# Performance work log

Measured on AMD Instinct MI355X. Metric: run time of the kernel, lower is better.

Reference implementation:

```python
import jax, jax.numpy as jnp
import numpy as np

HEAD_DIM = 64
SCALE = 1.0 / np.sqrt(HEAD_DIM).astype(np.float32)


def setup_inputs() -> dict:
    key = jax.random.key(0)
    k1, k2 = jax.random.split(key)
    B, S, D = 4, 4096, 1024
    x = jax.random.normal(k1, (B, S, D), dtype=jnp.float32)
    wq = jax.random.normal(k2, (HEAD_DIM, D), dtype=jnp.float32) * (1.0 / np.sqrt(D))
    return {"x": x, "wq": wq}


def reference(x, wq):
    # Faithful to the original forward: wq is (buggily) used for q, k AND v.
    q = jnp.einsum('bsd,hd->bsh', x, wq)   # [B, S, 64]
    k = q
    v = q
    scores = jnp.einsum('bqh,bkh->bqk', q, k) * SCALE  # [B, S, S]
    attn = jax.nn.softmax(scores, axis=-1)
    out = jnp.einsum('bqk,bkh->bqh', attn, v)          # [B, S, 64]
    return out
```

## Files before the change

### kernel.cpp

```cpp
#include <hip/hip_runtime.h>
#include <hip/hip_bf16.h>

#define B_ 4
#define S_ 4096
#define D_ 1024
#define H_ 64
#define SCALE_ 0.125f
#define CFAC_ 0.180336884f
#define WP_ 1056
#define SP_ 4224
#define NSPLIT 4

typedef __attribute__((ext_vector_type(8))) short bf16x8;
typedef __attribute__((ext_vector_type(4))) float f32x4;

static __device__ __forceinline__ short f2bf(float f) {
    unsigned u = __builtin_bit_cast(unsigned, f);
    u += 0x7fffu + ((u >> 16) & 1u);
    return (short)(u >> 16);
}

static __device__ __forceinline__ unsigned pk_trunc(float f0, float f1) {
    return (__builtin_bit_cast(unsigned, f1) & 0xffff0000u)
         | (__builtin_bit_cast(unsigned, f0) >> 16);
}

__global__ __launch_bounds__(256) void winit_kernel(
    const float* __restrict__ wq, short* __restrict__ wqb)
{
    const int i   = blockIdx.x * 256 + threadIdx.x;
    const int row = i >> 7;
    const int col = (i & 127) * 8;
    const float* s = wq + (size_t)row * D_ + col;
    bf16x8 v;
#pragma unroll
    for (int e = 0; e < 8; ++e) v[e] = f2bf(s[e]);
    *(bf16x8*)(wqb + (size_t)row * WP_ + col) = v;
}

__global__ __launch_bounds__(256) void qproj_mfma(
    const float* __restrict__ x, const short* __restrict__ wqb,
    short* __restrict__ q, short* __restrict__ qT, short* __restrict__ qsb)
{
    __shared__ short xs[4][16][264];
    __shared__ float cs[4][16][68];
    __shared__ short qs[16][68];

    const int tid  = threadIdx.x;
    const int wave = tid >> 6;
    const int lane = tid & 63;
    const int quad = lane >> 4;
    const int lr   = lane & 15;
    const int row0 = blockIdx.x * 16;

    {
        const float* xp = x + (size_t)row0 * D_ + wave * 256 + lane * 4;
#pragma unroll
        for (int s = 0; s < 16; ++s) {
            const f32x4 v = *(const f32x4*)(xp + (size_t)s * D_);
            unsigned long long pk = 0;
#pragma unroll
            for (int e = 0; e < 4; ++e)
                pk |= (unsigned long long)(unsigned short)f2bf(v[e]) << (16 * e);
            *(unsigned long long*)&xs[wave][s][lane * 4] = pk;
        }
    }
    __syncthreads();

    f32x4 acc[4];
#pragma unroll
    for (int nb = 0; nb < 4; ++nb) acc[nb] = (f32x4){0.f, 0.f, 0.f, 0.f};

    const short* wp = wqb + (size_t)lr * WP_ + wave * 256 + quad * 8;
#pragma unroll
    for (int t = 0; t < 8; ++t) {
        const bf16x8 a = *(const bf16x8*)&xs[wave][lr][t * 32 + quad * 8];
#pragma unroll
        for (int nb = 0; nb < 4; ++nb) {
            const bf16x8 bb = *(const bf16x8*)(wp + (size_t)(nb * 16) * WP_ + t * 32);
            acc[nb] = __builtin_amdgcn_mfma_f32_16x16x32_bf16(a, bb, acc[nb], 0, 0, 0);
        }
    }

#pragma unroll
    for (int nb = 0; nb < 4; ++nb)
#pragma unroll
        for (int i = 0; i < 4; ++i)
            cs[wave][quad * 4 + i][nb * 16 + lr] = acc[nb][i];
    __syncthreads();

    const int r  = tid >> 4;
    const int c4 = (tid & 15) * 4;
    unsigned long long pv = 0, pw = 0;
#pragma unroll
    for (int j = 0; j < 4; ++j) {
        const float s = cs[0][r][c4 + j] + cs[1][r][c4 + j]
                      + cs[2][r][c4 + j] + cs[3][r][c4 + j];
        pv |= (unsigned long long)(unsigned short)f2bf(s) << (16 * j);
        pw |= (unsigned long long)(unsigned short)f2bf(s * CFAC_) << (16 * j);
    }
    *(unsigned long long*)(q   + (size_t)(row0 + r) * H_ + c4) = pv;
    *(unsigned long long*)(qsb + (size_t)(row0 + r) * H_ + c4) = pw;
    *(unsigned long long*)&qs[r][c4] = pv;
    __syncthreads();

    const int hh = tid >> 2;
    const int sj = (tid & 3) * 4;
    const int b  = row0 >> 12;
    const int sl = row0 & (S_ - 1);
    unsigned long long w = 0;
#pragma unroll
    for (int e = 0; e < 4; ++e)
        w |= (unsigned long long)(unsigned short)qs[sj + e][hh] << (16 * e);
    *(unsigned long long*)(qT + ((size_t)b * H_ + hh) * SP_ + sl + sj) = w;
}

__global__ __launch_bounds__(256, 4) void flash_mfma(
    const short* __restrict__ q, const short* __restrict__ qT,
    const short* __restrict__ qsb,
    float* __restrict__ opart, float* __restrict__ lbuf)
{
    __shared__ short kt[64 * 64];
    __shared__ short vt[64 * 64];
    __shared__ short plT[4][16][72];

    const int tid  = threadIdx.x;
    const int w    = tid >> 6;
    const int lane = tid & 63;
    const int quad = lane >> 4;
    const int lr   = lane & 15;
    const int b    = blockIdx.y;
    const int q0   = blockIdx.x * 64;
    const int z    = blockIdx.z;
    const int slice = S_ / gridDim.z;
    const int kbase = z * slice;
    const short* qb  = q  + (size_t)b * S_ * H_;
    const short* qTb = qT + (size_t)b * H_ * SP_;

    bf16x8 qB[2];
    {
        const short* qr = qsb + (size_t)(b * S_ + q0 + w * 16 + lr) * H_;
        qB[0] = *(const bf16x8*)(qr + quad * 8);
        qB[1] = *(const bf16x8*)(qr + 32 + quad * 8);
    }

    bf16x8 ones;
#pragma unroll
    for (int e = 0; e < 8; ++e) ones[e] = (short)0x3f80;

    f32x4 o[4];
#pragma unroll
    for (int mt = 0; mt < 4; ++mt) o[mt] = (f32x4){0.f, 0.f, 0.f, 0.f};
    f32x4 lsum = (f32x4){0.f, 0.f, 0.f, 0.f};

    const int srow = tid >> 2;
    const int g0   = (tid & 3) * 2;
    const int sw0  = (g0 ^ (srow & 7)) * 8;
    const int sw1  = ((g0 + 1) ^ (srow & 7)) * 8;
    const short* gk = qb  + (size_t)(kbase + srow) * H_ + g0 * 8;
    const short* gv = qTb + (size_t)srow * SP_ + kbase + g0 * 8;

    uint4 pk0 = *(const uint4*)gk, pk1 = *(const uint4*)(gk + 8);
    uint4 pv0 = *(const uint4*)gv, pv1 = *(const uint4*)(gv + 8);

    const int iters = slice >> 6;
    for (int it = 0; it < iters; ++it) {
        __syncthreads();
        *(uint4*)&kt[srow * 64 + sw0] = pk0;
        *(uint4*)&kt[srow * 64 + sw1] = pk1;
        *(uint4*)&vt[srow * 64 + sw0] = pv0;
        *(uint4*)&vt[srow * 64 + sw1] = pv1;
        __syncthreads();
        if (it + 1 < iters) {
            gk += (size_t)64 * H_;
            gv += 64;
            pk0 = *(const uint4*)gk; pk1 = *(const uint4*)(gk + 8);
            pv0 = *(const uint4*)gv; pv1 = *(const uint4*)(gv + 8);
        }

        f32x4 s[4];
#pragma unroll
        for (int mt = 0; mt < 4; ++mt) s[mt] = (f32x4){0.f, 0.f, 0.f, 0.f};
#pragma unroll
        for (int c = 0; c < 2; ++c)
#pragma unroll
            for (int mt = 0; mt < 4; ++mt) {
                const int row = mt * 16 + lr;
                const bf16x8 a = *(const bf16x8*)&kt[row * 64 + (((c * 4 + quad) ^ (row & 7)) * 8)];
                s[mt] = __builtin_amdgcn_mfma_f32_16x16x32_bf16(a, qB[c], s[mt], 0, 0, 0);
            }

#pragma unroll
        for (int mt = 0; mt < 4; ++mt) {
            const float p0 = __builtin_amdgcn_exp2f(s[mt][0]);
            const float p1 = __builtin_amdgcn_exp2f(s[mt][1]);
            const float p2 = __builtin_amdgcn_exp2f(s[mt][2]);
            const float p3 = __builtin_amdgcn_exp2f(s[mt][3]);
            unsigned lohi[2];
            lohi[0] = pk_trunc(p0, p1);
            lohi[1] = pk_trunc(p2, p3);
            *(unsigned long long*)&plT[w][lr][mt * 16 + quad * 4] =
                *(unsigned long long*)lohi;
        }

#pragma unroll
        for (int c = 0; c < 2; ++c) {
            const bf16x8 pB = *(const bf16x8*)&plT[w][lr][c * 32 + quad * 8];
            lsum = __builtin_amdgcn_mfma_f32_16x16x32_bf16(ones, pB, lsum, 0, 0, 0);
#pragma unroll
            for (int mt = 0; mt < 4; ++mt) {
                const int row = mt * 16 + lr;
                const bf16x8 a = *(const bf16x8*)&vt[row * 64 + (((c * 4 + quad) ^ (row & 7)) * 8)];
                o[mt] = __builtin_amdgcn_mfma_f32_16x16x32_bf16(a, pB, o[mt], 0, 0, 0);
            }
        }
    }

    float* ob = opart + (((size_t)z * B_ + b) * S_ + q0 + w * 16 + lr) * H_;
#pragma unroll
    for (int mt = 0; mt < 4; ++mt)
        *(f32x4*)(ob + mt * 16 + quad * 4) = o[mt];
    if (quad == 0)
        lbuf[((size_t)z * B_ + b) * S_ + q0 + w * 16 + lr] = lsum[0];
}

__global__ __launch_bounds__(256) void combine_kernel(
    const float* __restrict__ opart, const float* __restrict__ lbuf,
    float* __restrict__ out, int nsplit)
{
    const int t   = blockIdx.x * 256 + threadIdx.x;
    const int row = t >> 4;
    const int c4  = (t & 15) * 4;
    f32x4 acc = (f32x4){0.f, 0.f, 0.f, 0.f};
    float l = 0.0f;
    for (int z = 0; z < nsplit; ++z) {
        const f32x4 v = *(const f32x4*)(opart + ((size_t)z * (B_ * S_) + row) * H_ + c4);
        acc[0] += v[0]; acc[1] += v[1]; acc[2] += v[2]; acc[3] += v[3];
        l += lbuf[(size_t)z * (B_ * S_) + row];
    }
    const float r = 1.0f / l;
    acc[0] *= r; acc[1] *= r; acc[2] *= r; acc[3] *= r;
    *(f32x4*)(out + (size_t)row * H_ + c4) = acc;
}

extern "C" void kernel_launch(void* const* d_in, const int* in_sizes, int n_in,
                              void* d_out, int out_size, void* d_ws, size_t ws_size,
                              hipStream_t stream) {
    const float* x  = (const float*)d_in[0];
    const float* wq = (const float*)d_in[1];
    float* out = (float*)d_out;

    const size_t off_qT  = 2097152;
    const size_t off_wqb = off_qT + (size_t)B_ * H_ * SP_ * 2;
    const size_t off_qsb = off_wqb + (size_t)H_ * WP_ * 2;
    const size_t off_op  = off_qsb + 2097152;
    short* qbuf = (short*)d_ws;
    short* qT   = (short*)((char*)d_ws + off_qT);
    short* wqb  = (short*)((char*)d_ws + off_wqb);
    short* qsb  = (short*)((char*)d_ws + off_qsb);

    const size_t per_split = (size_t)B_ * S_ * H_ * 4 + (size_t)B_ * S_ * 4;
    int nsplit = NSPLIT;
    while (nsplit > 1 && ws_size < off_op + (size_t)nsplit * per_split) nsplit >>= 1;
    float* opart = (float*)((char*)d_ws + off_op);
    float* lbuf  = (float*)((char*)d_ws + off_op + (size_t)nsplit * B_ * S_ * H_ * 4);

    winit_kernel<<<dim3(32), dim3(256), 0, stream>>>(wq, wqb);
    qproj_mfma<<<dim3((B_ * S_) / 16), dim3(256), 0, stream>>>(x, wqb, qbuf, qT, qsb);
    flash_mfma<<<dim3(S_ / 64, B_, nsplit), dim3(256), 0, stream>>>(qbuf, qT, qsb, opart, lbuf);
    combine_kernel<<<dim3(1024), dim3(256), 0, stream>>>(opart, lbuf, out, nsplit);
}
```

Before: 134.8 us.

## Process two query sub-tiles per wave to reuse K/V LDS tiles; double split count

Each flash block now covers 128 query rows instead of 64, with each wave handling two 16-row query sub-tiles that share the same K and V LDS fragments. This halves LDS loading and global K/V traffic per query row and raises the MFMA-to-load ratio. To keep the grid size the same, the key-dimension split goes from 4 to 8. That doubles the partial-output buffers and the work in the combine kernel, and the extra accumulators raise register pressure, which may hurt occupancy.

Result: no change. 134.6 us (-0.1%).

```diff
diff --git a/kernel.cpp b/kernel.cpp
--- a/kernel.cpp
+++ b/kernel.cpp
@@ -9,7 +9,7 @@
 #define CFAC_ 0.180336884f
 #define WP_ 1056
 #define SP_ 4224
-#define NSPLIT 4
+#define NSPLIT 8
 
 typedef __attribute__((ext_vector_type(8))) short bf16x8;
 typedef __attribute__((ext_vector_type(4))) float f32x4;
@@ -122,7 +122,7 @@
 {
     __shared__ short kt[64 * 64];
     __shared__ short vt[64 * 64];
-    __shared__ short plT[4][16][72];
+    __shared__ short plT[4][2][16][72];
 
     const int tid  = threadIdx.x;
     const int w    = tid >> 6;
@@ -130,28 +130,33 @@
     const int quad = lane >> 4;
     const int lr   = lane & 15;
     const int b    = blockIdx.y;
-    const int q0   = blockIdx.x * 64;
+    const int q0   = blockIdx.x * 128;
     const int z    = blockIdx.z;
     const int slice = S_ / gridDim.z;
     const int kbase = z * slice;
     const short* qb  = q  + (size_t)b * S_ * H_;
     const short* qTb = qT + (size_t)b * H_ * SP_;
 
-    bf16x8 qB[2];
-    {
-        const short* qr = qsb + (size_t)(b * S_ + q0 + w * 16 + lr) * H_;
-        qB[0] = *(const bf16x8*)(qr + quad * 8);
-        qB[1] = *(const bf16x8*)(qr + 32 + quad * 8);
+    bf16x8 qB[2][2];
+#pragma unroll
+    for (int qs = 0; qs < 2; ++qs) {
+        const short* qr = qsb + (size_t)(b * S_ + q0 + w * 32 + qs * 16 + lr) * H_;
+        qB[qs][0] = *(const bf16x8*)(qr + quad * 8);
+        qB[qs][1] = *(const bf16x8*)(qr + 32 + quad * 8);
     }
 
     bf16x8 ones;
 #pragma unroll
     for (int e = 0; e < 8; ++e) ones[e] = (short)0x3f80;
 
-    f32x4 o[4];
-#pragma unroll
-    for (int mt = 0; mt < 4; ++mt) o[mt] = (f32x4){0.f, 0.f, 0.f, 0.f};
-    f32x4 lsum = (f32x4){0.f, 0.f, 0.f, 0.f};
+    f32x4 o[2][4];
+#pragma unroll
+    for (int qs = 0; qs < 2; ++qs)
+#pragma unroll
+        for (int mt = 0; mt < 4; ++mt) o[qs][mt] = (f32x4){0.f, 0.f, 0.f, 0.f};
+    f32x4 lsum[2];
+    lsum[0] = (f32x4){0.f, 0.f, 0.f, 0.f};
+    lsum[1] = (f32x4){0.f, 0.f, 0.f, 0.f};
 
     const int srow = tid >> 2;
     const int g0   = (tid & 3) * 2;
@@ -178,50 +183,64 @@
             pv0 = *(const uint4*)gv; pv1 = *(const uint4*)(gv + 8);
         }
 
-        f32x4 s[4];
-#pragma unroll
-        for (int mt = 0; mt < 4; ++mt) s[mt] = (f32x4){0.f, 0.f, 0.f, 0.f};
-#pragma unroll
-        for (int c = 0; c < 2; ++c)
-#pragma unroll
-            for (int mt = 0; mt < 4; ++mt) {
-                const int row = mt * 16 + lr;
-                const bf16x8 a = *(const bf16x8*)&kt[row * 64 + (((c * 4 + quad) ^ (row & 7)) * 8)];
-                s[mt] = __builtin_amdgcn_mfma_f32_16x16x32_bf16(a, qB[c], s[mt], 0, 0, 0);
-            }
-
-#pragma unroll
-        for (int mt = 0; mt < 4; ++mt) {
-            const float p0 = __builtin_amdgcn_exp2f(s[mt][0]);
-            const float p1 = __builtin_amdgcn_exp2f(s[mt][1]);
-            const float p2 = __builtin_amdgcn_exp2f(s[mt][2]);
-            const float p3 = __builtin_amdgcn_exp2f(s[mt][3]);
-            unsigned lohi[2];
-            lohi[0] = pk_trunc(p0, p1);
-            lohi[1] = pk_trunc(p2, p3);
-            *(unsigned long long*)&plT[w][lr][mt * 16 + quad * 4] =
-                *(unsigned long long*)lohi;
+#pragma unroll
+        for (int mp = 0; mp < 2; ++mp) {
+            f32x4 s[2][2];
+            s[0][0] = (f32x4){0.f, 0.f, 0.f, 0.f};
+            s[0][1] = (f32x4){0.f, 0.f, 0.f, 0.f};
+            s[1][0] = (f32x4){0.f, 0.f, 0.f, 0.f};
+            s[1][1] = (f32x4){0.f, 0.f, 0.f, 0.f};
+#pragma unroll
+            for (int c = 0; c < 2; ++c)
+#pragma unroll
+                for (int m2 = 0; m2 < 2; ++m2) {
+                    const int row = (mp * 2 + m2) * 16 + lr;
+                    const bf16x8 a = *(const bf16x8*)&kt[row * 64 + (((c * 4 + quad) ^ (row & 7)) * 8)];
+                    s[0][m2] = __builtin_amdgcn_mfma_f32_16x16x32_bf16(a, qB[0][c], s[0][m2], 0, 0, 0);
+                    s[1][m2] = __builtin_amdgcn_mfma_f32_16x16x32_bf16(a, qB[1][c], s[1][m2], 0, 0, 0);
+                }
+#pragma unroll
+            for (int qs = 0; qs < 2; ++qs)
+#pragma unroll
+                for (int m2 = 0; m2 < 2; ++m2) {
+                    const int mt = mp * 2 + m2;
+                    const float p0 = __builtin_amdgcn_exp2f(s[qs][m2][0]);
+                    const float p1 = __builtin_amdgcn_exp2f(s[qs][m2][1]);
+                    const float p2 = __builtin_amdgcn_exp2f(s[qs][m2][2]);
+                    const float p3 = __builtin_amdgcn_exp2f(s[qs][m2][3]);
+                    unsigned lohi[2];
+                    lohi[0] = pk_trunc(p0, p1);
+                    lohi[1] = pk_trunc(p2, p3);
+                    *(unsigned long long*)&plT[w][qs][lr][mt * 16 + quad * 4] =
+                        *(unsigned long long*)lohi;
+                }
         }
 
 #pragma unroll
         for (int c = 0; c < 2; ++c) {
-            const bf16x8 pB = *(const bf16x8*)&plT[w][lr][c * 32 + quad * 8];
-            lsum = __builtin_amdgcn_mfma_f32_16x16x32_bf16(ones, pB, lsum, 0, 0, 0);
+            const bf16x8 pB0 = *(const bf16x8*)&plT[w][0][lr][c * 32 + quad * 8];
+            const bf16x8 pB1 = *(const bf16x8*)&plT[w][1][lr][c * 32 + quad * 8];
+            lsum[0] = __builtin_amdgcn_mfma_f32_16x16x32_bf16(ones, pB0, lsum[0], 0, 0, 0);
+            lsum[1] = __builtin_amdgcn_mfma_f32_16x16x32_bf16(ones, pB1, lsum[1], 0, 0, 0);
 #pragma unroll
             for (int mt = 0; mt < 4; ++mt) {
                 const int row = mt * 16 + lr;
                 const bf16x8 a = *(const bf16x8*)&vt[row * 64 + (((c * 4 + quad) ^ (row & 7)) * 8)];
-                o[mt] = __builtin_amdgcn_mfma_f32_16x16x32_bf16(a, pB, o[mt], 0, 0, 0);
+                o[0][mt] = __builtin_amdgcn_mfma_f32_16x16x32_bf16(a, pB0, o[0][mt], 0, 0, 0);
+                o[1][mt] = __builtin_amdgcn_mfma_f32_16x16x32_bf16(a, pB1, o[1][mt], 0, 0, 0);
             }
         }
     }
 
-    float* ob = opart + (((size_t)z * B_ + b) * S_ + q0 + w * 16 + lr) * H_;
-#pragma unroll
-    for (int mt = 0; mt < 4; ++mt)
-        *(f32x4*)(ob + mt * 16 + quad * 4) = o[mt];
-    if (quad == 0)
-        lbuf[((size_t)z * B_ + b) * S_ + q0 + w * 16 + lr] = lsum[0];
+#pragma unroll
+    for (int qs = 0; qs < 2; ++qs) {
+        float* ob = opart + (((size_t)z * B_ + b) * S_ + q0 + w * 32 + qs * 16 + lr) * H_;
+#pragma unroll
+        for (int mt = 0; mt < 4; ++mt)
+            *(f32x4*)(ob + mt * 16 + quad * 4) = o[qs][mt];
+        if (quad == 0)
+            lbuf[((size_t)z * B_ + b) * S_ + q0 + w * 32 + qs * 16 + lr] = lsum[qs][0];
+    }
 }
 
 __global__ __launch_bounds__(256) void combine_kernel(
@@ -267,6 +286,6 @@
 
     winit_kernel<<<dim3(32), dim3(256), 0, stream>>>(wq, wqb);
     qproj_mfma<<<dim3((B_ * S_) / 16), dim3(256), 0, stream>>>(x, wqb, qbuf, qT, qsb);
-    flash_mfma<<<dim3(S_ / 64, B_, nsplit), dim3(256), 0, stream>>>(qbuf, qT, qsb, opart, lbuf);
+    flash_mfma<<<dim3(S_ / 128, B_, nsplit), dim3(256), 0, stream>>>(qbuf, qT, qsb, opart, lbuf);
     combine_kernel<<<dim3(1024), dim3(256), 0, stream>>>(opart, lbuf, out, nsplit);
 }
```
